# Performance work log

Hardware: AMD Instinct MI355X
Metric: run time of the kernel (lower is better)

Reference implementation:

```python
import jax, jax.numpy as jnp
import numpy as np

WEIGHT = 0.1
NEIGHBORHOOD_SIZE = 3
EPSILON = 1e-06


def setup_inputs() -> dict:
    key = jax.random.key(0)
    x = jax.random.normal(key, (8, 3, 1024, 1024), dtype=jnp.float32)
    return {"x": x}


def reference(x):
    b, c, h, w = x.shape
    total = jnp.zeros((), dtype=x.dtype)
    for k in range(-NEIGHBORHOOD_SIZE, NEIGHBORHOOD_SIZE + 1):
        for l in range(-NEIGHBORHOOD_SIZE, NEIGHBORHOOD_SIZE + 1):
            if k == 0 and l == 0:
                continue
            shifted = jnp.roll(x, shift=(k, l), axis=(2, 3))
            diff = jnp.abs(x - shifted)
            total = total + jnp.sqrt(diff * diff + EPSILON).sum()
    return WEIGHT * total / (b * c * h * w)
```

## Files before the change

kernel.cpp:

```cpp
#include <hip/hip_runtime.h>


#define HDIM 1024
#define WDIM 1024
#define PLANES 24
#define MASK 1023
#define NTOT (PLANES * HDIM * WDIM)
#define RROWS 32
#define BPP (HDIM / RROWS)
#define NBLOCKS (PLANES * BPP)
#define NGROUPS (RROWS / 4)

typedef __attribute__((address_space(1))) const float gfloat_t;
typedef __attribute__((address_space(3))) float lfloat_t;

__global__ __launch_bounds__(256) void btv_main(const float* __restrict__ x,
                                                float* __restrict__ partial) {
    __shared__ float lds[12][WDIM];

    const int plane  = blockIdx.x / BPP;
    const int istart = (blockIdx.x % BPP) * RROWS;
    const int tid = threadIdx.x;
    const int j  = tid << 2;
    const int cl = (j - 4) & MASK;
    const int cr = (j + 4) & MASK;
    const float* pbase = x + (size_t)plane * (HDIM * WDIM);
    const int woff = (tid & 0xC0) << 2;

    const float* pA = &lds[0][0];
    const float* pB = &lds[4][0];
    const float* pC = &lds[8][0];

#define STAGE(g, PTRC) do {                                              \
        _Pragma("unroll")                                                \
        for (int i2 = 0; i2 < 4; ++i2) {                                 \
            const int row_ = (istart + 4 * (g) + i2) & MASK;             \
            const float* gp_ = pbase + (size_t)row_ * WDIM + j;          \
            __builtin_amdgcn_global_load_lds((gfloat_t*)gp_,             \
                (lfloat_t*)((PTRC) + i2 * WDIM + woff), 16, 0, 0);       \
        }                                                                \
    } while (0)

#define READ_ROW(S, PTR, LOCAL) do {                                     \
        const float* rp_ = (PTR) + (LOCAL) * WDIM;                       \
        float4 a_ = *(const float4*)(rp_ + cl);                          \
        float4 b_ = *(const float4*)(rp_ + j);                           \
        float4 c_ = *(const float4*)(rp_ + cr);                          \
        w[S][0] = a_.x; w[S][1] = a_.y; w[S][2]  = a_.z; w[S][3]  = a_.w;\
        w[S][4] = b_.x; w[S][5] = b_.y; w[S][6]  = b_.z; w[S][7]  = b_.w;\
        w[S][8] = c_.x; w[S][9] = c_.y; w[S][10] = c_.z; w[S][11] = c_.w;\
    } while (0)

#define COMPUTE(I) do {                                                  \
        const int s0 = (I) & 3, s1 = ((I) + 1) & 3,                      \
                  s2 = ((I) + 2) & 3, s3 = ((I) + 3) & 3;                \
        _Pragma("unroll")                                                \
        for (int p = 0; p < 4; ++p) {                                    \
            const float own = w[s0][4 + p];                              \
            float a = __builtin_fabsf(own - w[s0][5 + p]);               \
            a += __builtin_fabsf(own - w[s0][6 + p]);                    \
            a += __builtin_fabsf(own - w[s0][7 + p]);                    \
            _Pragma("unroll")                                            \
            for (int l = -3; l <= 3; ++l)                                \
                a += __builtin_fabsf(own - w[s1][4 + p + l]);            \
            _Pragma("unroll")                                            \
            for (int l = -3; l <= 3; ++l)                                \
                a += __builtin_fabsf(own - w[s2][4 + p + l]);            \
            _Pragma("unroll")                                            \
            for (int l = -3; l <= 3; ++l)                                \
                a += __builtin_fabsf(own - w[s3][4 + p + l]);            \
            acc[p] += a;                                                 \
        }                                                                \
    } while (0)

    STAGE(0, pA);
    STAGE(1, pB);
    __syncthreads();

    float w[4][12];
    READ_ROW(0, pA, 0);
    READ_ROW(1, pA, 1);
    READ_ROW(2, pA, 2);

    float acc[4] = {0.f, 0.f, 0.f, 0.f};

    for (int c = 0; c < NGROUPS; ++c) {
        if (c) __syncthreads();
        if (c <= NGROUPS - 2) STAGE(c + 2, pC);
        READ_ROW(3, pA, 3); COMPUTE(0);
        READ_ROW(0, pB, 0); COMPUTE(1);
        READ_ROW(1, pB, 1); COMPUTE(2);
        READ_ROW(2, pB, 2); COMPUTE(3);
        const float* t_ = pA; pA = pB; pB = pC; pC = t_;
    }

#undef STAGE
#undef READ_ROW
#undef COMPUTE

    float acct = (acc[0] + acc[1]) + (acc[2] + acc[3]);

#pragma unroll
    for (int off = 32; off > 0; off >>= 1)
        acct += __shfl_down(acct, off, 64);

    __shared__ float s[4];
    const int lane = tid & 63;
    const int wid  = tid >> 6;
    if (lane == 0) s[wid] = acct;
    __syncthreads();
    if (tid == 0)
        partial[blockIdx.x] = (s[0] + s[1]) + (s[2] + s[3]);
}

__global__ __launch_bounds__(256) void btv_fin(const float* __restrict__ partial,
                                               float* __restrict__ out) {
    double s = 0.0;
    for (int i = threadIdx.x; i < NBLOCKS; i += 256)
        s += (double)partial[i];
#pragma unroll
    for (int off = 32; off > 0; off >>= 1)
        s += __shfl_down(s, off, 64);
    __shared__ double sh[4];
    const int lane = threadIdx.x & 63;
    const int wid  = threadIdx.x >> 6;
    if (lane == 0) sh[wid] = s;
    __syncthreads();
    if (threadIdx.x == 0) {
        double t = (sh[0] + sh[1]) + (sh[2] + sh[3]);
        *out = (float)(t * (0.2 / (double)NTOT));
    }
}

extern "C" void kernel_launch(void* const* d_in, const int* in_sizes, int n_in,
                              void* d_out, int out_size, void* d_ws, size_t ws_size,
                              hipStream_t stream) {
    const float* x = (const float*)d_in[0];
    float* out = (float*)d_out;
    float* partial = (float*)d_ws;

    btv_main<<<NBLOCKS, 256, 0, stream>>>(x, partial);
    btv_fin<<<1, 256, 0, stream>>>(partial, out);
}
```

Baseline: 167.8 us.

## Replace LDS-staged rows with direct global loads and 8-wide per-thread columns

Drops the global_load_lds staging into shared memory, its barriers and the triple buffering. Each thread now loads its row window straight from global memory into registers and handles 8 columns instead of 4. Blocks shrink to 128 threads and strips to 16 rows, which doubles the block count. The goal is to remove LDS traffic and synchronisation and to raise arithmetic per load. In exchange, overlapping halo loads now hit L1/L2 instead of LDS, each strip re-reads more halo rows, and register pressure goes up.

After: 188.7 us. 1.13x slower.

```diff
diff --git a/kernel.cpp b/kernel.cpp
--- a/kernel.cpp
+++ b/kernel.cpp
@@ -6,56 +6,47 @@
 #define PLANES 24
 #define MASK 1023
 #define NTOT (PLANES * HDIM * WDIM)
-#define RROWS 32
-#define BPP (HDIM / RROWS)
-#define NBLOCKS (PLANES * BPP)
+#define RROWS 16
+#define SPP (HDIM / RROWS)
+#define NBLOCKS (PLANES * SPP)
 #define NGROUPS (RROWS / 4)
 
-typedef __attribute__((address_space(1))) const float gfloat_t;
-typedef __attribute__((address_space(3))) float lfloat_t;
+__global__ __launch_bounds__(128) void btv_main(const float* __restrict__ x,
+                                                float* __restrict__ partial) {
+    const int strip  = blockIdx.x;
+    const int plane  = strip >> 6;
+    const int istart = (strip & (SPP - 1)) * RROWS;
+    const int tid = threadIdx.x;
+    const int j  = tid << 3;
+    const int c0 = (j - 4) & MASK;
+    const int c1 = j;
+    const int c2 = (j + 4) & MASK;
+    const int c3 = (j + 8) & MASK;
+    const float* pbase = x + (size_t)plane * (HDIM * WDIM);
 
-__global__ __launch_bounds__(256) void btv_main(const float* __restrict__ x,
-                                                float* __restrict__ partial) {
-    __shared__ float lds[12][WDIM];
+    float w[4][16];
 
-    const int plane  = blockIdx.x / BPP;
-    const int istart = (blockIdx.x % BPP) * RROWS;
-    const int tid = threadIdx.x;
-    const int j  = tid << 2;
-    const int cl = (j - 4) & MASK;
-    const int cr = (j + 4) & MASK;
-    const float* pbase = x + (size_t)plane * (HDIM * WDIM);
-    const int woff = (tid & 0xC0) << 2;
-
-    const float* pA = &lds[0][0];
-    const float* pB = &lds[4][0];
-    const float* pC = &lds[8][0];
-
-#define STAGE(g, PTRC) do {                                              \
-        _Pragma("unroll")                                                \
-        for (int i2 = 0; i2 < 4; ++i2) {                                 \
-            const int row_ = (istart + 4 * (g) + i2) & MASK;             \
-            const float* gp_ = pbase + (size_t)row_ * WDIM + j;          \
-            __builtin_amdgcn_global_load_lds((gfloat_t*)gp_,             \
-                (lfloat_t*)((PTRC) + i2 * WDIM + woff), 16, 0, 0);       \
-        }                                                                \
-    } while (0)
-
-#define READ_ROW(S, PTR, LOCAL) do {                                     \
-        const float* rp_ = (PTR) + (LOCAL) * WDIM;                       \
-        float4 a_ = *(const float4*)(rp_ + cl);                          \
-        float4 b_ = *(const float4*)(rp_ + j);                           \
-        float4 c_ = *(const float4*)(rp_ + cr);                          \
-        w[S][0] = a_.x; w[S][1] = a_.y; w[S][2]  = a_.z; w[S][3]  = a_.w;\
-        w[S][4] = b_.x; w[S][5] = b_.y; w[S][6]  = b_.z; w[S][7]  = b_.w;\
-        w[S][8] = c_.x; w[S][9] = c_.y; w[S][10] = c_.z; w[S][11] = c_.w;\
+#define LOAD_ROW(slot, m) do {                                           \
+        const float* rb_ = pbase + (((m) & MASK) * WDIM);                \
+        float4 q0_ = *(const float4*)(rb_ + c0);                         \
+        float4 q1_ = *(const float4*)(rb_ + c1);                         \
+        float4 q2_ = *(const float4*)(rb_ + c2);                         \
+        float4 q3_ = *(const float4*)(rb_ + c3);                         \
+        w[slot][0]  = q0_.x; w[slot][1]  = q0_.y;                        \
+        w[slot][2]  = q0_.z; w[slot][3]  = q0_.w;                        \
+        w[slot][4]  = q1_.x; w[slot][5]  = q1_.y;                        \
+        w[slot][6]  = q1_.z; w[slot][7]  = q1_.w;                        \
+        w[slot][8]  = q2_.x; w[slot][9]  = q2_.y;                        \
+        w[slot][10] = q2_.z; w[slot][11] = q2_.w;                        \
+        w[slot][12] = q3_.x; w[slot][13] = q3_.y;                        \
+        w[slot][14] = q3_.z; w[slot][15] = q3_.w;                        \
     } while (0)
 
 #define COMPUTE(I) do {                                                  \
         const int s0 = (I) & 3, s1 = ((I) + 1) & 3,                      \
                   s2 = ((I) + 2) & 3, s3 = ((I) + 3) & 3;                \
         _Pragma("unroll")                                                \
-        for (int p = 0; p < 4; ++p) {                                    \
+        for (int p = 0; p < 8; ++p) {                                    \
             const float own = w[s0][4 + p];                              \
             float a = __builtin_fabsf(own - w[s0][5 + p]);               \
             a += __builtin_fabsf(own - w[s0][6 + p]);                    \
@@ -73,44 +64,37 @@
         }                                                                \
     } while (0)
 
-    STAGE(0, pA);
-    STAGE(1, pB);
-    __syncthreads();
+    LOAD_ROW(0, istart + 0);
+    LOAD_ROW(1, istart + 1);
+    LOAD_ROW(2, istart + 2);
 
-    float w[4][12];
-    READ_ROW(0, pA, 0);
-    READ_ROW(1, pA, 1);
-    READ_ROW(2, pA, 2);
+    float acc[8] = {0.f, 0.f, 0.f, 0.f, 0.f, 0.f, 0.f, 0.f};
 
-    float acc[4] = {0.f, 0.f, 0.f, 0.f};
-
+#pragma unroll 1
     for (int c = 0; c < NGROUPS; ++c) {
-        if (c) __syncthreads();
-        if (c <= NGROUPS - 2) STAGE(c + 2, pC);
-        READ_ROW(3, pA, 3); COMPUTE(0);
-        READ_ROW(0, pB, 0); COMPUTE(1);
-        READ_ROW(1, pB, 1); COMPUTE(2);
-        READ_ROW(2, pB, 2); COMPUTE(3);
-        const float* t_ = pA; pA = pB; pB = pC; pC = t_;
+        const int rbase = istart + 4 * c;
+#pragma unroll
+        for (int i = 0; i < 4; ++i) {
+            LOAD_ROW((i + 3) & 3, rbase + i + 3);
+            COMPUTE(i);
+        }
     }
 
-#undef STAGE
-#undef READ_ROW
+#undef LOAD_ROW
 #undef COMPUTE
 
-    float acct = (acc[0] + acc[1]) + (acc[2] + acc[3]);
+    float acct = ((acc[0] + acc[1]) + (acc[2] + acc[3])) +
+                 ((acc[4] + acc[5]) + (acc[6] + acc[7]));
 
 #pragma unroll
     for (int off = 32; off > 0; off >>= 1)
         acct += __shfl_down(acct, off, 64);
 
-    __shared__ float s[4];
-    const int lane = tid & 63;
-    const int wid  = tid >> 6;
-    if (lane == 0) s[wid] = acct;
+    __shared__ float s[2];
+    if ((tid & 63) == 0) s[tid >> 6] = acct;
     __syncthreads();
     if (tid == 0)
-        partial[blockIdx.x] = (s[0] + s[1]) + (s[2] + s[3]);
+        partial[blockIdx.x] = s[0] + s[1];
 }
 
 __global__ __launch_bounds__(256) void btv_fin(const float* __restrict__ partial,
@@ -139,6 +123,6 @@
     float* out = (float*)d_out;
     float* partial = (float*)d_ws;
 
-    btv_main<<<NBLOCKS, 256, 0, stream>>>(x, partial);
+    btv_main<<<NBLOCKS, 128, 0, stream>>>(x, partial);
     btv_fin<<<1, 256, 0, stream>>>(partial, out);
 }
```
